# Kernel optimization log

Hardware: AMD Instinct MI355X
Metric: run time of the kernel (lower is better)

## Reference

```python
import jax, jax.numpy as jnp
import numpy as np

N, E = 3000, 48000
FEAT, HID, OUT = 32, 32, 8
R, K, N_CONV = 2, 5, 2
RATIO = 0.9  # TopKPooling ratio


def _glorot(key, o, i):
    return jax.random.normal(key, (o, i), jnp.float32) * (1.0 / np.sqrt(i))


def setup_inputs() -> dict:
    key = jax.random.key(0)
    ks = jax.random.split(key, 13)
    x = jax.random.normal(ks[0], (N, FEAT), jnp.float32)
    row = jax.random.randint(ks[1], (E,), 0, N, dtype=jnp.int32)
    col = jax.random.randint(ks[2], (E,), 0, N, dtype=jnp.int32)
    col = jnp.where(col == row, (col + 1) % N, col)  # no self loops
    edge_index = jnp.stack([row, col])
    return {
        "x": x,
        "edge_index": edge_index,
        "h": jnp.float32(0.5),       # learnable zoom parameter
        "alpha": jnp.float32(0.1),   # learnable spectral shift
        "Wr0": _glorot(ks[3], HID, FEAT),
        "Wc0a": _glorot(ks[4], HID, FEAT),  # Re(ComplexLinear.weight); Im part never reaches the output
        "Wc0b": _glorot(ks[5], HID, FEAT),
        "Wr1": _glorot(ks[6], HID, HID),
        "Wc1a": _glorot(ks[7], HID, HID),
        "Wc1b": _glorot(ks[8], HID, HID),
        "pool_w": jax.random.normal(ks[9], (HID,), jnp.float32),
        "lin_weight": _glorot(ks[10], OUT, HID),
        "lin_bias": jax.random.normal(ks[11], (OUT,), jnp.float32) * 0.01,
    }


def _cayley_conv(x, edge_index, h, alpha, Wr, Wcs):
    # Dense Jacobi iteration approximating the Cayley spectral filter.
    # The original builds 2n x 2n block matrices [[T,0],[0,B]] whose off-
    # diagonal blocks are zero and whose bottom-half state starts at (and
    # provably stays) zero, so we compute the identical top block only and
    # append the zero bottom half at the end (matching the (2n, C) output).
    n = x.shape[0]
    row, col = edge_index[0], edge_index[1]
    deg = jnp.zeros((n,), x.dtype).at[row].add(1.0)            # scatter-add degree
    A = jnp.zeros((n, n), x.dtype).at[row, col].set(1.0)       # dense adjacency (set, like L[row,col]=w)
    idx = jnp.arange(n)
    dvals = deg - alpha                                        # shifted Laplacian diagonal
    L = (-A).at[idx, idx].set(dvals)                           # L = D - A - alpha*I, dense
    Off = L.at[idx, idx].set(0.0)                              # off-diagonal part (NOT scaled by h)
    invD = 1.0 / (dvals * h)                                   # inverse of diag(h*L)
    b_mat = invD[:, None] * (h * L)                            # extended_tmp_Dia @ extended_tmp_right (top block)
    J = -(Off * invD[None, :])                                 # jacobi = -Off @ D^{-1} (top block)
    out = x @ Wr.T                                             # real_linear([x;0]) top half
    y = x
    for Wc in Wcs:                                             # r polynomial orders
        b_j = b_mat @ y
        yk = b_j
        for _ in range(K):                                     # K Jacobi iterations
            yk = J @ yk + b_j
        y = yk
        out = out + 2.0 * (y @ Wc.T)                           # 2*Re(ComplexLinear(y)), y real => only Re(W) contributes
    return jnp.concatenate([out, jnp.zeros_like(out)], axis=0)  # (2n, C_out)


def reference(x, edge_index, h, alpha, Wr0, Wc0a, Wc0b, Wr1, Wc1a, Wc1b, pool_w, lin_weight, lin_bias):
    x1 = jax.nn.relu(_cayley_conv(x, edge_index, h, alpha, Wr0, [Wc0a, Wc0b]))
    x2 = jax.nn.relu(_cayley_conv(x1, edge_index, h, alpha, Wr1, [Wc1a, Wc1b]))
    n_total = x2.shape[0]                      # 4N: each conv doubles node count
    k = int(np.ceil(RATIO * n_total))          # TopKPooling(ratio=0.9), static k
    score = jnp.tanh((x2 @ pool_w) / jnp.linalg.norm(pool_w))
    vals, perm = jax.lax.top_k(score, k)
    xp = x2[perm] * vals[:, None]              # gate selected nodes by tanh-score
    g = jnp.mean(xp, axis=0)                   # global_mean_pool (single graph)
    # dropout(p=0.2) is identity in eval mode
    return (g @ lin_weight.T + lin_bias)[None, :]  # (1, OUT)
```

## Files before the change

### kernel.cpp

```cpp
#include <hip/hip_runtime.h>
#include <hip/hip_bf16.h>

typedef __hip_bfloat16 bf16;
typedef unsigned short u16;
typedef unsigned int   u32;

#define NN 3000
#define EE 48000
#define NF 32
#define KEXC 1200
#define KDEN 10800.0f
#define NB 32
#define NT 1024
#define CT 1024
#define SEG 94
#define CS  47
#define SLOTS 48128
#define DUMMYC 3070u
#define PADROW 3071u
#define FLUSHB 0x40000000u
#define PARTB  0x80000000u

#define OFF_CNT  0u
#define OFF_TOT  128u
#define OFF_EXC  256u
#define OFF_SLOT 512u
#define OFF_WINV 193024u
#define OFF_XT   205056u
#define OFF_Y1   589056u
#define OFF_Y2   973056u
#define OFF_X1T  1357056u
#define OFF_X2T  1741056u

__device__ __forceinline__ bool scalar_is_bf16(const void* hp) {
    return ((const unsigned short*)hp)[0] != 0x0000;
}
__device__ __forceinline__ bool tensor_is_bf16(const void* xp) {
    const unsigned short* u = (const unsigned short*)xp;
    int cnt = 0;
    for (int k = 0; k < 16; k++) {
        unsigned e = (u[2 * k] >> 7) & 0xFF;
        if (e >= 107 && e <= 147) cnt++;
    }
    return cnt >= 12;
}
__device__ __forceinline__ float ldv(const void* p, int i, bool b16) {
    return b16 ? __bfloat162float(((const bf16*)p)[i]) : ((const float*)p)[i];
}

__global__ void __launch_bounds__(NT)
k_csr(const int* __restrict__ ei, const void* __restrict__ x,
      const void* hp, const void* ap,
      float* __restrict__ winv, u32* __restrict__ slotT,
      float* __restrict__ xT, u32* __restrict__ zhdr) {
    __shared__ u16 tmp_c[4096], tmp_r[4096];
    __shared__ u16 stage[4096], rid[4096];
    __shared__ int s_deg[128], sA[128];
    __shared__ int lcur[96];
    __shared__ int s_base, s_cnt;
    __shared__ int s_fl[2];
    const int t = threadIdx.x, blk = blockIdx.x;

    if (t == 0) {
        s_fl[0] = scalar_is_bf16(hp) ? 1 : 0;
        s_fl[1] = tensor_is_bf16(x) ? 1 : 0;
        s_base = 0; s_cnt = 0;
    }
    if (blk == 0 && t < 96) zhdr[t] = 0u;
    if (t < 128) s_deg[t] = 0;
    if (t < 96) lcur[t] = 0;
    __syncthreads();
    const bool sbf = s_fl[0] != 0, xtb = s_fl[1] != 0;
    const float hh = ldv(hp, 0, sbf), aa = ldv(ap, 0, sbf);

    const int r0 = blk * SEG;
    const int r1 = (r0 + SEG < NN) ? (r0 + SEG) : NN;

    for (int idx = t; idx < SEG * NF; idx += NT) {
        int f = idx / SEG, ii = idx % SEG;
        int i = r0 + ii;
        if (i < NN) xT[f * NN + i] = ldv(x, i * NF + f, xtb);
    }

    int cntlt = 0;
    for (int e = t; e < EE; e += NT) {
        int r = ei[e];
        if (r >= r0 && r < r1) {
            int p = atomicAdd(&s_cnt, 1);
            tmp_c[p] = (u16)ei[EE + e];
            tmp_r[p] = (u16)(r - r0);
            atomicAdd(&s_deg[r - r0], 1);
        } else {
            cntlt += (r < r0) ? 1 : 0;
        }
    }
#pragma unroll
    for (int o = 32; o > 0; o >>= 1) cntlt += __shfl_down(cntlt, o);
    if ((t & 63) == 0 && cntlt) atomicAdd(&s_base, cntlt);
    __syncthreads();
    const int base = s_base;
    const int cnt  = s_cnt;

    if (t < r1 - r0)
        winv[r0 + t] = 1.0f / (hh * ((float)s_deg[t] - aa));

    if (t < 96) sA[t] = s_deg[t];
    __syncthreads();
#pragma unroll
    for (int d = 1; d < 96; d <<= 1) {
        int v = 0;
        if (t < 96) v = sA[t] + ((t >= d) ? sA[t - d] : 0);
        __syncthreads();
        if (t < 96) sA[t] = v;
        __syncthreads();
    }
#define LPEX(rr) ((rr) == 0 ? 0 : sA[(rr) - 1])

    for (int l = t; l < cnt; l += NT) {
        int rr = tmp_r[l];
        int pos = atomicAdd(&lcur[rr], 1);
        stage[LPEX(rr) + pos] = tmp_c[l];
    }
    __syncthreads();
    for (int rr = t; rr < (r1 - r0); rr += NT) {
        int s0 = LPEX(rr), s1 = LPEX(rr + 1);
        for (int s2 = s0; s2 < s1; s2++) rid[s2] = (u16)rr;
    }
    __syncthreads();
    for (int ls = t; ls < cnt; ls += NT) {
        int rr = rid[ls];
        int rs = LPEX(rr);
        u16 c = stage[ls];
        bool dup = false;
        for (int ls2 = rs; ls2 < ls; ls2++) dup |= (stage[ls2] == c);
        if (dup) stage[ls] = (u16)DUMMYC;
    }
    __syncthreads();
    for (int ls = t; ls < cnt; ls += NT) {
        int rr = rid[ls];
        int s = base + ls;
        int rs = base + LPEX(rr), re = base + LPEX(rr + 1);
        int tc = s / CS, j = s % CS;
        bool atEnd = (s == re - 1), atRange = (j == CS - 1);
        bool flush = atEnd || atRange;
        int frag = tc - rs / CS; if (frag > 3) frag = 3;
        u32 pidx = ((u32)(r0 + rr) << 2) | (u32)frag;
        u32 p = (u32)stage[ls] | (pidx << 12)
              | (flush ? FLUSHB : 0u);
        slotT[j * CT + tc] = p;
    }
    if (blk == 31) {
        for (int s = EE + t; s < SLOTS; s += NT) {
            int tc = s / CS, j = s % CS;
            slotT[j * CT + tc] = DUMMYC | ((PADROW << 2) << 12)
                               | ((j == CS - 1) ? FLUSHB : 0u);
        }
    }
#undef LPEX
}

__global__ void __launch_bounds__(CT, 1)
k_chains(const float* __restrict__ xinT, const void* hp,
         const u32* __restrict__ slotT, const float* __restrict__ winv,
         float* __restrict__ y1g, float* __restrict__ y2g) {
    __shared__ float s_y[3072], s_sys[3072], s_b[3072], s_w[3072];
    __shared__ float s_part[3072 * 4];
    __shared__ int s_fl[1];
    const int t = threadIdx.x, blk = blockIdx.x;

    if (t == 0) s_fl[0] = scalar_is_bf16(hp) ? 1 : 0;
    __syncthreads();
    const float hh = ldv(hp, 0, s_fl[0] != 0);

    u32 sl[CS];
#pragma unroll
    for (int j = 0; j < CS; j++) sl[j] = slotT[j * CT + t];

#pragma unroll
    for (int k = 0; k < 3; k++) {
        int i = t + k * CT;
        float v = (i < NN) ? xinT[blk * NN + i] : 0.0f;
        float w = (i < NN) ? winv[i] : 0.0f;
        s_w[i] = w; s_y[i] = v; s_sys[i] = w * v;
    }
    for (int i = t; i < 3072 * 4; i += CT) s_part[i] = 0.0f;
    __syncthreads();

#pragma unroll 1
    for (int ord = 0; ord < 2; ord++) {
#pragma unroll 1
        for (int step = 0; step < 6; step++) {
            const float* src = (step == 0) ? s_y : s_sys;
            float acc = 0.f;
#pragma unroll
            for (int s = 0; s < CS; s++) {
                u32 p = sl[s];
                acc += src[p & 0xFFFu];
                if (p & FLUSHB) {
                    s_part[(p >> 12) & 0x3FFFu] = acc;
                    acc = 0.f;
                }
            }
            __syncthreads();
            if (step == 0) {
#pragma unroll
                for (int k = 0; k < 3; k++) {
                    int i = t + k * CT;
                    const float4 pr = *(const float4*)&s_part[i * 4];
                    float a = (pr.x + pr.y) + (pr.z + pr.w);
                    float nb = s_y[i] - hh * s_w[i] * a;
                    s_b[i] = nb; s_y[i] = nb; s_sys[i] = s_w[i] * nb;
                }
            } else {
#pragma unroll
                for (int k = 0; k < 3; k++) {
                    int i = t + k * CT;
                    const float4 pr = *(const float4*)&s_part[i * 4];
                    float a = (pr.x + pr.y) + (pr.z + pr.w);
                    float y = s_b[i] + a;
                    s_y[i] = y; s_sys[i] = s_w[i] * y;
                }
            }
            __syncthreads();
        }
        float* yg = (ord == 0) ? y1g : y2g;
#pragma unroll
        for (int k = 0; k < 3; k++) {
            int i = t + k * CT;
            if (i < NN) yg[blk * NN + i] = s_y[i];
        }
    }
}

__global__ void __launch_bounds__(256)
k_gemmT(const float* __restrict__ xinT,
        const void* __restrict__ Wr, const void* __restrict__ Wa, const void* __restrict__ Wb,
        const float* __restrict__ y1T, const float* __restrict__ y2T,
        float* __restrict__ outT) {
    __shared__ float sW[96];
    __shared__ int s_fl;
    const int t = threadIdx.x, o = blockIdx.y;
    if (t == 0) s_fl = tensor_is_bf16(Wr) ? 1 : 0;
    __syncthreads();
    const bool wtb = s_fl != 0;
    if (t < 96) {
        sW[t] = (t < 32) ? ldv(Wr, o * 32 + t, wtb)
              : (t < 64) ? 2.0f * ldv(Wa, o * 32 + (t - 32), wtb)
                         : 2.0f * ldv(Wb, o * 32 + (t - 64), wtb);
    }
    __syncthreads();
    int i = blockIdx.x * 256 + t;
    if (i >= NN) return;
    float acc = 0.f;
#pragma unroll
    for (int f = 0; f < NF; f++)
        acc += xinT[f * NN + i] * sW[f]
             + y1T[f * NN + i] * sW[32 + f]
             + y2T[f * NN + i] * sW[64 + f];
    outT[o * NN + i] = fmaxf(acc, 0.f);
}

__global__ void __launch_bounds__(512)
k_pool(const float* __restrict__ x2T, const void* __restrict__ pwp,
       const void* __restrict__ lwp, const void* __restrict__ lbp,
       u32* __restrict__ cntg, float* __restrict__ totf, float* __restrict__ excf,
       void* __restrict__ outp) {
    __shared__ float s_s[3072];
    __shared__ float red[512];
    __shared__ int rnk[96];
    __shared__ int s_fl, s_last;
    const int t = threadIdx.x, blk = blockIdx.x;
    const int PNT = 512;

    if (t == 0) s_fl = tensor_is_bf16(pwp) ? 1 : 0;
    __syncthreads();
    const bool tb = s_fl != 0;
    float pw[32];
    float nrm2 = 0.f;
#pragma unroll
    for (int f = 0; f < NF; f++) { pw[f] = ldv(pwp, f, tb); nrm2 += pw[f] * pw[f]; }
    const float nrm = sqrtf(nrm2);

    for (int i = t; i < 3072; i += PNT) {
        if (i < NN) {
            float d = 0.f;
#pragma unroll
            for (int f = 0; f < NF; f++) d += x2T[f * NN + i] * pw[f];
            s_s[i] = tanhf(d / nrm);
        } else s_s[i] = 0.f;
    }
    if (t < 96) rnk[t] = 0;
    __syncthreads();

    const int j0 = blk * SEG;
    const int j1 = (j0 + SEG < NN) ? (j0 + SEG) : NN;
    for (int u = t; u < SEG * 5; u += PNT) {
        int lr = u / 5, i = j0 + lr;
        if (i < j1) {
            float si = s_s[i];
            if (si < 0.f) {
                int seg = (u % 5) * 600;
                int c2 = 0;
                for (int j = seg; j < seg + 600 && j < NN; j++) {
                    float sj = s_s[j];
                    c2 += (sj < si) || ((sj == si) && (j > i));
                }
                if (c2) atomicAdd(&rnk[lr], c2);
            }
        }
    }
    __syncthreads();

    int f = t & 31, rl = t >> 5;
    float at = 0.f, ae = 0.f;
    for (int lr = rl; lr < SEG; lr += 16) {
        int i = j0 + lr;
        if (i < j1) {
            float si = s_s[i];
            float term = x2T[f * NN + i] * si;
            at += term;
            if (si < 0.f && rnk[lr] < KEXC) ae += term;
        }
    }
    red[t] = at; __syncthreads();
    for (int s = 256; s >= 32; s >>= 1) { if (t < s) red[t] += red[t + s]; __syncthreads(); }
    if (t < 32) atomicAdd(&totf[t], red[t]);
    __syncthreads();
    red[t] = ae; __syncthreads();
    for (int s = 256; s >= 32; s >>= 1) { if (t < s) red[t] += red[t + s]; __syncthreads(); }
    if (t < 32) atomicAdd(&excf[t], red[t]);
    __syncthreads();

    if (t == 0) {
        __threadfence();
        u32 old = atomicAdd(cntg, 1u);
        s_last = (old == NB - 1) ? 1 : 0;
    }
    __syncthreads();
    if (s_last) {
        __threadfence();
        if (t < 8) {
            float o = ldv(lbp, t, tb);
            for (int ff = 0; ff < NF; ff++) {
                float tv = __hip_atomic_load(&totf[ff], __ATOMIC_RELAXED, __HIP_MEMORY_SCOPE_AGENT);
                float ev = __hip_atomic_load(&excf[ff], __ATOMIC_RELAXED, __HIP_MEMORY_SCOPE_AGENT);
                o += ((tv - ev) / KDEN) * ldv(lwp, t * 32 + ff, tb);
            }
            if (tb) ((bf16*)outp)[t] = __float2bfloat16(o);
            else    ((float*)outp)[t] = o;
        }
    }
}

extern "C" void kernel_launch(void* const* d_in, const int* in_sizes, int n_in,
                              void* d_out, int out_size, void* d_ws, size_t ws_size,
                              hipStream_t stream) {
    const void* x   = d_in[0];
    const int*  ei  = (const int*)d_in[1];
    const void* hp  = d_in[2];
    const void* ap  = d_in[3];
    const void* Wr0 = d_in[4];
    const void* Wa0 = d_in[5];
    const void* Wb0 = d_in[6];
    const void* Wr1 = d_in[7];
    const void* Wa1 = d_in[8];
    const void* Wb1 = d_in[9];
    const void* pw  = d_in[10];
    const void* lw  = d_in[11];
    const void* lb  = d_in[12];
    char* ws = (char*)d_ws;

    u32*   cntg  = (u32*)(ws + OFF_CNT);
    float* totf  = (float*)(ws + OFF_TOT);
    float* excf  = (float*)(ws + OFF_EXC);
    u32*   slotT = (u32*)(ws + OFF_SLOT);
    float* winv  = (float*)(ws + OFF_WINV);
    float* xT    = (float*)(ws + OFF_XT);
    float* y1g   = (float*)(ws + OFF_Y1);
    float* y2g   = (float*)(ws + OFF_Y2);
    float* x1T   = (float*)(ws + OFF_X1T);
    float* x2T   = (float*)(ws + OFF_X2T);

    k_csr   <<<dim3(32),     dim3(NT),  0, stream>>>(ei, x, hp, ap, winv, slotT, xT, (u32*)ws);
    k_chains<<<dim3(32),     dim3(CT),  0, stream>>>(xT, hp, slotT, winv, y1g, y2g);
    k_gemmT <<<dim3(12, 32), dim3(256), 0, stream>>>(xT, Wr0, Wa0, Wb0, y1g, y2g, x1T);
    k_chains<<<dim3(32),     dim3(CT),  0, stream>>>(x1T, hp, slotT, winv, y1g, y2g);
    k_gemmT <<<dim3(12, 32), dim3(256), 0, stream>>>(x1T, Wr1, Wa1, Wb1, y1g, y2g, x2T);
    k_pool  <<<dim3(32),     dim3(512), 0, stream>>>(x2T, pw, lw, lb, cntg, totf, excf, d_out);
}
```

Before: 259.3 us.

## Fuse all six kernels into one cooperative persistent kernel with grid syncs

Replaces the CSR build, two chain solves, two feature GEMMs and the pooling kernels with a single cooperative launch of 32 blocks of 1024 threads. Grid-wide syncs separate the phases, and a shared-memory union lets the phases reuse LDS. This removes five kernel launch gaps and the last-block atomic counter. In exchange, the GEMM and pooling phases now run on only 32 blocks instead of 384 and 32×512 threads, and each grid.sync adds its own cost.

Result: slower. 478.9 us (+84.7%).

```diff
diff --git a/kernel.cpp b/kernel.cpp
--- a/kernel.cpp
+++ b/kernel.cpp
@@ -1,5 +1,8 @@
 #include <hip/hip_runtime.h>
 #include <hip/hip_bf16.h>
+#include <hip/hip_cooperative_groups.h>
+
+namespace cg = cooperative_groups;
 
 typedef __hip_bfloat16 bf16;
 typedef unsigned short u16;
@@ -19,9 +22,7 @@
 #define DUMMYC 3070u
 #define PADROW 3071u
 #define FLUSHB 0x40000000u
-#define PARTB  0x80000000u
-
-#define OFF_CNT  0u
+
 #define OFF_TOT  128u
 #define OFF_EXC  256u
 #define OFF_SLOT 512u
@@ -48,130 +49,30 @@
     return b16 ? __bfloat162float(((const bf16*)p)[i]) : ((const float*)p)[i];
 }
 
-__global__ void __launch_bounds__(NT)
-k_csr(const int* __restrict__ ei, const void* __restrict__ x,
-      const void* hp, const void* ap,
-      float* __restrict__ winv, u32* __restrict__ slotT,
-      float* __restrict__ xT, u32* __restrict__ zhdr) {
-    __shared__ u16 tmp_c[4096], tmp_r[4096];
-    __shared__ u16 stage[4096], rid[4096];
-    __shared__ int s_deg[128], sA[128];
-    __shared__ int lcur[96];
-    __shared__ int s_base, s_cnt;
-    __shared__ int s_fl[2];
-    const int t = threadIdx.x, blk = blockIdx.x;
-
-    if (t == 0) {
-        s_fl[0] = scalar_is_bf16(hp) ? 1 : 0;
-        s_fl[1] = tensor_is_bf16(x) ? 1 : 0;
-        s_base = 0; s_cnt = 0;
-    }
-    if (blk == 0 && t < 96) zhdr[t] = 0u;
-    if (t < 128) s_deg[t] = 0;
-    if (t < 96) lcur[t] = 0;
-    __syncthreads();
-    const bool sbf = s_fl[0] != 0, xtb = s_fl[1] != 0;
-    const float hh = ldv(hp, 0, sbf), aa = ldv(ap, 0, sbf);
-
-    const int r0 = blk * SEG;
-    const int r1 = (r0 + SEG < NN) ? (r0 + SEG) : NN;
-
-    for (int idx = t; idx < SEG * NF; idx += NT) {
-        int f = idx / SEG, ii = idx % SEG;
-        int i = r0 + ii;
-        if (i < NN) xT[f * NN + i] = ldv(x, i * NF + f, xtb);
-    }
-
-    int cntlt = 0;
-    for (int e = t; e < EE; e += NT) {
-        int r = ei[e];
-        if (r >= r0 && r < r1) {
-            int p = atomicAdd(&s_cnt, 1);
-            tmp_c[p] = (u16)ei[EE + e];
-            tmp_r[p] = (u16)(r - r0);
-            atomicAdd(&s_deg[r - r0], 1);
-        } else {
-            cntlt += (r < r0) ? 1 : 0;
-        }
-    }
-#pragma unroll
-    for (int o = 32; o > 0; o >>= 1) cntlt += __shfl_down(cntlt, o);
-    if ((t & 63) == 0 && cntlt) atomicAdd(&s_base, cntlt);
-    __syncthreads();
-    const int base = s_base;
-    const int cnt  = s_cnt;
-
-    if (t < r1 - r0)
-        winv[r0 + t] = 1.0f / (hh * ((float)s_deg[t] - aa));
-
-    if (t < 96) sA[t] = s_deg[t];
-    __syncthreads();
-#pragma unroll
-    for (int d = 1; d < 96; d <<= 1) {
-        int v = 0;
-        if (t < 96) v = sA[t] + ((t >= d) ? sA[t - d] : 0);
-        __syncthreads();
-        if (t < 96) sA[t] = v;
-        __syncthreads();
-    }
-#define LPEX(rr) ((rr) == 0 ? 0 : sA[(rr) - 1])
-
-    for (int l = t; l < cnt; l += NT) {
-        int rr = tmp_r[l];
-        int pos = atomicAdd(&lcur[rr], 1);
-        stage[LPEX(rr) + pos] = tmp_c[l];
-    }
-    __syncthreads();
-    for (int rr = t; rr < (r1 - r0); rr += NT) {
-        int s0 = LPEX(rr), s1 = LPEX(rr + 1);
-        for (int s2 = s0; s2 < s1; s2++) rid[s2] = (u16)rr;
-    }
-    __syncthreads();
-    for (int ls = t; ls < cnt; ls += NT) {
-        int rr = rid[ls];
-        int rs = LPEX(rr);
-        u16 c = stage[ls];
-        bool dup = false;
-        for (int ls2 = rs; ls2 < ls; ls2++) dup |= (stage[ls2] == c);
-        if (dup) stage[ls] = (u16)DUMMYC;
-    }
-    __syncthreads();
-    for (int ls = t; ls < cnt; ls += NT) {
-        int rr = rid[ls];
-        int s = base + ls;
-        int rs = base + LPEX(rr), re = base + LPEX(rr + 1);
-        int tc = s / CS, j = s % CS;
-        bool atEnd = (s == re - 1), atRange = (j == CS - 1);
-        bool flush = atEnd || atRange;
-        int frag = tc - rs / CS; if (frag > 3) frag = 3;
-        u32 pidx = ((u32)(r0 + rr) << 2) | (u32)frag;
-        u32 p = (u32)stage[ls] | (pidx << 12)
-              | (flush ? FLUSHB : 0u);
-        slotT[j * CT + tc] = p;
-    }
-    if (blk == 31) {
-        for (int s = EE + t; s < SLOTS; s += NT) {
-            int tc = s / CS, j = s % CS;
-            slotT[j * CT + tc] = DUMMYC | ((PADROW << 2) << 12)
-                               | ((j == CS - 1) ? FLUSHB : 0u);
-        }
-    }
-#undef LPEX
-}
-
-__global__ void __launch_bounds__(CT, 1)
-k_chains(const float* __restrict__ xinT, const void* hp,
-         const u32* __restrict__ slotT, const float* __restrict__ winv,
-         float* __restrict__ y1g, float* __restrict__ y2g) {
-    __shared__ float s_y[3072], s_sys[3072], s_b[3072], s_w[3072];
-    __shared__ float s_part[3072 * 4];
-    __shared__ int s_fl[1];
-    const int t = threadIdx.x, blk = blockIdx.x;
-
-    if (t == 0) s_fl[0] = scalar_is_bf16(hp) ? 1 : 0;
-    __syncthreads();
-    const float hh = ldv(hp, 0, s_fl[0] != 0);
-
+union SharedU {
+    struct {
+        float y[3072], sys[3072], b[3072], w[3072];
+        float part[3072 * 4];
+    } ch;
+    struct {
+        u16 tmp_c[4096], tmp_r[4096], stage[4096], rid[4096];
+        int deg[128], sA[128], lcur[96];
+        int base, cnt;
+    } cs;
+    struct {
+        float s_s[3072];
+        float red[1024];
+        int rnk[96];
+    } pl;
+};
+
+__device__ __forceinline__ void chains_body(
+    float* s_y, float* s_sys, float* s_b, float* s_w, float* s_part,
+    const float* __restrict__ xinT, const float hh,
+    const u32* __restrict__ slotT, const float* __restrict__ winv,
+    float* __restrict__ y1g, float* __restrict__ y2g,
+    const int t, const int blk)
+{
     u32 sl[CS];
 #pragma unroll
     for (int j = 0; j < CS; j++) sl[j] = slotT[j * CT + t];
@@ -232,123 +133,261 @@
     }
 }
 
-__global__ void __launch_bounds__(256)
-k_gemmT(const float* __restrict__ xinT,
-        const void* __restrict__ Wr, const void* __restrict__ Wa, const void* __restrict__ Wb,
-        const float* __restrict__ y1T, const float* __restrict__ y2T,
-        float* __restrict__ outT) {
+__global__ void __launch_bounds__(NT, 4)
+k_fused(const int* __restrict__ ei, const void* __restrict__ x,
+        const void* hp, const void* ap,
+        const void* __restrict__ Wr0, const void* __restrict__ Wa0, const void* __restrict__ Wb0,
+        const void* __restrict__ Wr1, const void* __restrict__ Wa1, const void* __restrict__ Wb1,
+        const void* __restrict__ pwp, const void* __restrict__ lwp, const void* __restrict__ lbp,
+        void* __restrict__ outp, char* __restrict__ ws)
+{
+    __shared__ SharedU u;
     __shared__ float sW[96];
-    __shared__ int s_fl;
-    const int t = threadIdx.x, o = blockIdx.y;
-    if (t == 0) s_fl = tensor_is_bf16(Wr) ? 1 : 0;
-    __syncthreads();
-    const bool wtb = s_fl != 0;
-    if (t < 96) {
-        sW[t] = (t < 32) ? ldv(Wr, o * 32 + t, wtb)
-              : (t < 64) ? 2.0f * ldv(Wa, o * 32 + (t - 32), wtb)
-                         : 2.0f * ldv(Wb, o * 32 + (t - 64), wtb);
-    }
-    __syncthreads();
-    int i = blockIdx.x * 256 + t;
-    if (i >= NN) return;
-    float acc = 0.f;
-#pragma unroll
-    for (int f = 0; f < NF; f++)
-        acc += xinT[f * NN + i] * sW[f]
-             + y1T[f * NN + i] * sW[32 + f]
-             + y2T[f * NN + i] * sW[64 + f];
-    outT[o * NN + i] = fmaxf(acc, 0.f);
-}
-
-__global__ void __launch_bounds__(512)
-k_pool(const float* __restrict__ x2T, const void* __restrict__ pwp,
-       const void* __restrict__ lwp, const void* __restrict__ lbp,
-       u32* __restrict__ cntg, float* __restrict__ totf, float* __restrict__ excf,
-       void* __restrict__ outp) {
-    __shared__ float s_s[3072];
-    __shared__ float red[512];
-    __shared__ int rnk[96];
-    __shared__ int s_fl, s_last;
+    __shared__ int s_fl[2], s_gfl;
     const int t = threadIdx.x, blk = blockIdx.x;
-    const int PNT = 512;
-
-    if (t == 0) s_fl = tensor_is_bf16(pwp) ? 1 : 0;
-    __syncthreads();
-    const bool tb = s_fl != 0;
-    float pw[32];
-    float nrm2 = 0.f;
-#pragma unroll
-    for (int f = 0; f < NF; f++) { pw[f] = ldv(pwp, f, tb); nrm2 += pw[f] * pw[f]; }
-    const float nrm = sqrtf(nrm2);
-
-    for (int i = t; i < 3072; i += PNT) {
-        if (i < NN) {
-            float d = 0.f;
-#pragma unroll
-            for (int f = 0; f < NF; f++) d += x2T[f * NN + i] * pw[f];
-            s_s[i] = tanhf(d / nrm);
-        } else s_s[i] = 0.f;
-    }
-    if (t < 96) rnk[t] = 0;
-    __syncthreads();
-
-    const int j0 = blk * SEG;
-    const int j1 = (j0 + SEG < NN) ? (j0 + SEG) : NN;
-    for (int u = t; u < SEG * 5; u += PNT) {
-        int lr = u / 5, i = j0 + lr;
-        if (i < j1) {
-            float si = s_s[i];
-            if (si < 0.f) {
-                int seg = (u % 5) * 600;
-                int c2 = 0;
-                for (int j = seg; j < seg + 600 && j < NN; j++) {
-                    float sj = s_s[j];
-                    c2 += (sj < si) || ((sj == si) && (j > i));
+    cg::grid_group grid = cg::this_grid();
+
+    float* totf  = (float*)(ws + OFF_TOT);
+    float* excf  = (float*)(ws + OFF_EXC);
+    u32*   slotT = (u32*)(ws + OFF_SLOT);
+    float* winv  = (float*)(ws + OFF_WINV);
+    float* xT    = (float*)(ws + OFF_XT);
+    float* y1g   = (float*)(ws + OFF_Y1);
+    float* y2g   = (float*)(ws + OFF_Y2);
+    float* x1T   = (float*)(ws + OFF_X1T);
+    float* x2T   = (float*)(ws + OFF_X2T);
+
+    {
+        if (t == 0) {
+            s_fl[0] = scalar_is_bf16(hp) ? 1 : 0;
+            s_fl[1] = tensor_is_bf16(x) ? 1 : 0;
+            u.cs.base = 0; u.cs.cnt = 0;
+        }
+        if (blk == 0 && t < 96) ((u32*)ws)[t] = 0u;
+        if (t < 128) u.cs.deg[t] = 0;
+        if (t < 96) u.cs.lcur[t] = 0;
+        __syncthreads();
+        const bool sbf = s_fl[0] != 0, xtb = s_fl[1] != 0;
+        const float hh = ldv(hp, 0, sbf), aa = ldv(ap, 0, sbf);
+
+        const int r0 = blk * SEG;
+        const int r1 = (r0 + SEG < NN) ? (r0 + SEG) : NN;
+
+        for (int idx = t; idx < SEG * NF; idx += NT) {
+            int f = idx / SEG, ii = idx % SEG;
+            int i = r0 + ii;
+            if (i < NN) xT[f * NN + i] = ldv(x, i * NF + f, xtb);
+        }
+
+        int cntlt = 0;
+        for (int e = t; e < EE; e += NT) {
+            int r = ei[e];
+            if (r >= r0 && r < r1) {
+                int p = atomicAdd(&u.cs.cnt, 1);
+                u.cs.tmp_c[p] = (u16)ei[EE + e];
+                u.cs.tmp_r[p] = (u16)(r - r0);
+                atomicAdd(&u.cs.deg[r - r0], 1);
+            } else {
+                cntlt += (r < r0) ? 1 : 0;
+            }
+        }
+#pragma unroll
+        for (int o = 32; o > 0; o >>= 1) cntlt += __shfl_down(cntlt, o);
+        if ((t & 63) == 0 && cntlt) atomicAdd(&u.cs.base, cntlt);
+        __syncthreads();
+        const int base = u.cs.base;
+        const int cnt  = u.cs.cnt;
+
+        if (t < r1 - r0)
+            winv[r0 + t] = 1.0f / (hh * ((float)u.cs.deg[t] - aa));
+
+        if (t < 96) u.cs.sA[t] = u.cs.deg[t];
+        __syncthreads();
+#pragma unroll
+        for (int d = 1; d < 96; d <<= 1) {
+            int v = 0;
+            if (t < 96) v = u.cs.sA[t] + ((t >= d) ? u.cs.sA[t - d] : 0);
+            __syncthreads();
+            if (t < 96) u.cs.sA[t] = v;
+            __syncthreads();
+        }
+#define LPEX(rr) ((rr) == 0 ? 0 : u.cs.sA[(rr) - 1])
+
+        for (int l = t; l < cnt; l += NT) {
+            int rr = u.cs.tmp_r[l];
+            int pos = atomicAdd(&u.cs.lcur[rr], 1);
+            u.cs.stage[LPEX(rr) + pos] = u.cs.tmp_c[l];
+        }
+        __syncthreads();
+        for (int rr = t; rr < (r1 - r0); rr += NT) {
+            int s0 = LPEX(rr), s1 = LPEX(rr + 1);
+            for (int s2 = s0; s2 < s1; s2++) u.cs.rid[s2] = (u16)rr;
+        }
+        __syncthreads();
+        for (int ls = t; ls < cnt; ls += NT) {
+            int rr = u.cs.rid[ls];
+            int rs = LPEX(rr);
+            u16 c = u.cs.stage[ls];
+            bool dup = false;
+            for (int ls2 = rs; ls2 < ls; ls2++) dup |= (u.cs.stage[ls2] == c);
+            if (dup) u.cs.stage[ls] = (u16)DUMMYC;
+        }
+        __syncthreads();
+        for (int ls = t; ls < cnt; ls += NT) {
+            int rr = u.cs.rid[ls];
+            int s = base + ls;
+            int rs = base + LPEX(rr), re = base + LPEX(rr + 1);
+            int tc = s / CS, j = s % CS;
+            bool atEnd = (s == re - 1), atRange = (j == CS - 1);
+            bool flush = atEnd || atRange;
+            int frag = tc - rs / CS; if (frag > 3) frag = 3;
+            u32 pidx = ((u32)(r0 + rr) << 2) | (u32)frag;
+            u32 p = (u32)u.cs.stage[ls] | (pidx << 12)
+                  | (flush ? FLUSHB : 0u);
+            slotT[j * CT + tc] = p;
+        }
+        if (blk == 31) {
+            for (int s = EE + t; s < SLOTS; s += NT) {
+                int tc = s / CS, j = s % CS;
+                slotT[j * CT + tc] = DUMMYC | ((PADROW << 2) << 12)
+                                   | ((j == CS - 1) ? FLUSHB : 0u);
+            }
+        }
+#undef LPEX
+    }
+    grid.sync();
+
+    const float hh = ldv(hp, 0, s_fl[0] != 0);
+
+    chains_body(u.ch.y, u.ch.sys, u.ch.b, u.ch.w, u.ch.part,
+                xT, hh, slotT, winv, y1g, y2g, t, blk);
+    grid.sync();
+
+    {
+        if (t == 0) s_gfl = tensor_is_bf16(Wr0) ? 1 : 0;
+        __syncthreads();
+        const bool wtb = s_gfl != 0;
+        if (t < 96) {
+            sW[t] = (t < 32) ? ldv(Wr0, blk * 32 + t, wtb)
+                  : (t < 64) ? 2.0f * ldv(Wa0, blk * 32 + (t - 32), wtb)
+                             : 2.0f * ldv(Wb0, blk * 32 + (t - 64), wtb);
+        }
+        __syncthreads();
+#pragma unroll
+        for (int k = 0; k < 3; k++) {
+            int i = t + k * CT;
+            if (i < NN) {
+                float acc = 0.f;
+#pragma unroll
+                for (int f = 0; f < NF; f++)
+                    acc += xT[f * NN + i] * sW[f]
+                         + y1g[f * NN + i] * sW[32 + f]
+                         + y2g[f * NN + i] * sW[64 + f];
+                x1T[blk * NN + i] = fmaxf(acc, 0.f);
+            }
+        }
+    }
+    grid.sync();
+
+    chains_body(u.ch.y, u.ch.sys, u.ch.b, u.ch.w, u.ch.part,
+                x1T, hh, slotT, winv, y1g, y2g, t, blk);
+    grid.sync();
+
+    {
+        __syncthreads();
+        if (t == 0) s_gfl = tensor_is_bf16(Wr1) ? 1 : 0;
+        __syncthreads();
+        const bool wtb = s_gfl != 0;
+        if (t < 96) {
+            sW[t] = (t < 32) ? ldv(Wr1, blk * 32 + t, wtb)
+                  : (t < 64) ? 2.0f * ldv(Wa1, blk * 32 + (t - 32), wtb)
+                             : 2.0f * ldv(Wb1, blk * 32 + (t - 64), wtb);
+        }
+        __syncthreads();
+#pragma unroll
+        for (int k = 0; k < 3; k++) {
+            int i = t + k * CT;
+            if (i < NN) {
+                float acc = 0.f;
+#pragma unroll
+                for (int f = 0; f < NF; f++)
+                    acc += x1T[f * NN + i] * sW[f]
+                         + y1g[f * NN + i] * sW[32 + f]
+                         + y2g[f * NN + i] * sW[64 + f];
+                x2T[blk * NN + i] = fmaxf(acc, 0.f);
+            }
+        }
+    }
+    grid.sync();
+
+    {
+        if (t == 0) s_gfl = tensor_is_bf16(pwp) ? 1 : 0;
+        __syncthreads();
+        const bool tb = s_gfl != 0;
+        float pw[32];
+        float nrm2 = 0.f;
+#pragma unroll
+        for (int f = 0; f < NF; f++) { pw[f] = ldv(pwp, f, tb); nrm2 += pw[f] * pw[f]; }
+        const float nrm = sqrtf(nrm2);
+
+        for (int i = t; i < 3072; i += NT) {
+            if (i < NN) {
+                float d = 0.f;
+#pragma unroll
+                for (int f = 0; f < NF; f++) d += x2T[f * NN + i] * pw[f];
+                u.pl.s_s[i] = tanhf(d / nrm);
+            } else u.pl.s_s[i] = 0.f;
+        }
+        if (t < 96) u.pl.rnk[t] = 0;
+        __syncthreads();
+
+        const int j0 = blk * SEG;
+        const int j1 = (j0 + SEG < NN) ? (j0 + SEG) : NN;
+        for (int uu = t; uu < SEG * 5; uu += NT) {
+            int lr = uu / 5, i = j0 + lr;
+            if (i < j1) {
+                float si = u.pl.s_s[i];
+                if (si < 0.f) {
+                    int seg = (uu % 5) * 600;
+                    int c2 = 0;
+                    for (int j = seg; j < seg + 600 && j < NN; j++) {
+                        float sj = u.pl.s_s[j];
+                        c2 += (sj < si) || ((sj == si) && (j > i));
+                    }
+                    if (c2) atomicAdd(&u.pl.rnk[lr], c2);
                 }
-                if (c2) atomicAdd(&rnk[lr], c2);
-            }
-        }
-    }
-    __syncthreads();
-
-    int f = t & 31, rl = t >> 5;
-    float at = 0.f, ae = 0.f;
-    for (int lr = rl; lr < SEG; lr += 16) {
-        int i = j0 + lr;
-        if (i < j1) {
-            float si = s_s[i];
-            float term = x2T[f * NN + i] * si;
-            at += term;
-            if (si < 0.f && rnk[lr] < KEXC) ae += term;
-        }
-    }
-    red[t] = at; __syncthreads();
-    for (int s = 256; s >= 32; s >>= 1) { if (t < s) red[t] += red[t + s]; __syncthreads(); }
-    if (t < 32) atomicAdd(&totf[t], red[t]);
-    __syncthreads();
-    red[t] = ae; __syncthreads();
-    for (int s = 256; s >= 32; s >>= 1) { if (t < s) red[t] += red[t + s]; __syncthreads(); }
-    if (t < 32) atomicAdd(&excf[t], red[t]);
-    __syncthreads();
-
-    if (t == 0) {
-        __threadfence();
-        u32 old = atomicAdd(cntg, 1u);
-        s_last = (old == NB - 1) ? 1 : 0;
-    }
-    __syncthreads();
-    if (s_last) {
-        __threadfence();
-        if (t < 8) {
-            float o = ldv(lbp, t, tb);
-            for (int ff = 0; ff < NF; ff++) {
-                float tv = __hip_atomic_load(&totf[ff], __ATOMIC_RELAXED, __HIP_MEMORY_SCOPE_AGENT);
-                float ev = __hip_atomic_load(&excf[ff], __ATOMIC_RELAXED, __HIP_MEMORY_SCOPE_AGENT);
-                o += ((tv - ev) / KDEN) * ldv(lwp, t * 32 + ff, tb);
-            }
-            if (tb) ((bf16*)outp)[t] = __float2bfloat16(o);
-            else    ((float*)outp)[t] = o;
-        }
+            }
+        }
+        __syncthreads();
+
+        int f = t & 31, rl = t >> 5;
+        float at = 0.f, ae = 0.f;
+        for (int lr = rl; lr < SEG; lr += 32) {
+            int i = j0 + lr;
+            if (i < j1) {
+                float si = u.pl.s_s[i];
+                float term = x2T[f * NN + i] * si;
+                at += term;
+                if (si < 0.f && u.pl.rnk[lr] < KEXC) ae += term;
+            }
+        }
+        u.pl.red[t] = at; __syncthreads();
+        for (int s = 512; s >= 32; s >>= 1) { if (t < s) u.pl.red[t] += u.pl.red[t + s]; __syncthreads(); }
+        if (t < 32) atomicAdd(&totf[t], u.pl.red[t]);
+        __syncthreads();
+        u.pl.red[t] = ae; __syncthreads();
+        for (int s = 512; s >= 32; s >>= 1) { if (t < s) u.pl.red[t] += u.pl.red[t + s]; __syncthreads(); }
+        if (t < 32) atomicAdd(&excf[t], u.pl.red[t]);
+    }
+    grid.sync();
+
+    if (blk == 0 && t < 8) {
+        const bool tb = s_gfl != 0;
+        float o = ldv(lbp, t, tb);
+        for (int ff = 0; ff < NF; ff++)
+            o += ((totf[ff] - excf[ff]) / KDEN) * ldv(lwp, t * 32 + ff, tb);
+        if (tb) ((bf16*)outp)[t] = __float2bfloat16(o);
+        else    ((float*)outp)[t] = o;
     }
 }
 
@@ -369,22 +408,15 @@
     const void* lw  = d_in[11];
     const void* lb  = d_in[12];
     char* ws = (char*)d_ws;
-
-    u32*   cntg  = (u32*)(ws + OFF_CNT);
-    float* totf  = (float*)(ws + OFF_TOT);
-    float* excf  = (float*)(ws + OFF_EXC);
-    u32*   slotT = (u32*)(ws + OFF_SLOT);
-    float* winv  = (float*)(ws + OFF_WINV);
-    float* xT    = (float*)(ws + OFF_XT);
-    float* y1g   = (float*)(ws + OFF_Y1);
-    float* y2g   = (float*)(ws + OFF_Y2);
-    float* x1T   = (float*)(ws + OFF_X1T);
-    float* x2T   = (float*)(ws + OFF_X2T);
-
-    k_csr   <<<dim3(32),     dim3(NT),  0, stream>>>(ei, x, hp, ap, winv, slotT, xT, (u32*)ws);
-    k_chains<<<dim3(32),     dim3(CT),  0, stream>>>(xT, hp, slotT, winv, y1g, y2g);
-    k_gemmT <<<dim3(12, 32), dim3(256), 0, stream>>>(xT, Wr0, Wa0, Wb0, y1g, y2g, x1T);
-    k_chains<<<dim3(32),     dim3(CT),  0, stream>>>(x1T, hp, slotT, winv, y1g, y2g);
-    k_gemmT <<<dim3(12, 32), dim3(256), 0, stream>>>(x1T, Wr1, Wa1, Wb1, y1g, y2g, x2T);
-    k_pool  <<<dim3(32),     dim3(512), 0, stream>>>(x2T, pw, lw, lb, cntg, totf, excf, d_out);
-}
+    void* outp = d_out;
+
+    void* args[] = {
+        (void*)&ei, (void*)&x, (void*)&hp, (void*)&ap,
+        (void*)&Wr0, (void*)&Wa0, (void*)&Wb0,
+        (void*)&Wr1, (void*)&Wa1, (void*)&Wb1,
+        (void*)&pw, (void*)&lw, (void*)&lb,
+        (void*)&outp, (void*)&ws
+    };
+    hipLaunchCooperativeKernel((void*)k_fused, dim3(NB), dim3(NT),
+                               args, 0, stream);
+}
```
